# Optimization experiments

Measured on AMD Instinct MI355X. Metric: run time of the kernel, lower is better.

The kernel has to match this reference:

```python
import jax, jax.numpy as jnp
import numpy as np

H = 16          # n_self_heads
CHUNK = 256     # chunk_size in chunk_gate_retention
GLN = 16.0      # gate_logit_normalizer
EPS = 1e-5      # norm_eps


def _rope_interleaved(t, cos, sin):
    # t: [B,T,H,hd]; cos,sin: [T,hd//2]; interleaved pairs (even, odd)
    x1 = t[..., 0::2]
    x2 = t[..., 1::2]
    c = cos[None, :, None, :]
    s = sin[None, :, None, :]
    r1 = x1 * c - x2 * s
    r2 = x1 * s + x2 * c
    return jnp.stack([r1, r2], axis=-1).reshape(t.shape)


def setup_inputs() -> dict:
    key = jax.random.key(0)
    ks = jax.random.split(key, 8)
    B, T, D = 2, 4096, 2048
    hd = D // H
    sc = D ** -0.5
    x = jax.random.normal(ks[0], (B, T, D), jnp.float32)
    # real rotary tables (interleaved), [T, hd//2]
    inv_freq = 1.0 / (10000.0 ** (np.arange(0, hd, 2, dtype=np.float32) / hd))
    ang = np.outer(np.arange(T, dtype=np.float32), inv_freq)
    cos = jnp.asarray(np.cos(ang))
    sin = jnp.asarray(np.sin(ang))
    Wq = jax.random.normal(ks[1], (D, D), jnp.float32) * sc
    Wk = jax.random.normal(ks[2], (D, D), jnp.float32) * sc
    Wv = jax.random.normal(ks[3], (D, D), jnp.float32) * sc
    Wg = jax.random.normal(ks[4], (D, D), jnp.float32) * sc
    Wgt = jax.random.normal(ks[5], (D, H), jnp.float32) * sc
    Wout = jax.random.normal(ks[6], (D, D), jnp.float32) * sc
    return {"x": x, "cos": cos, "sin": sin, "Wq": Wq, "Wk": Wk, "Wv": Wv,
            "Wg": Wg, "Wgt": Wgt, "Wout": Wout}


def reference(x, cos, sin, Wq, Wk, Wv, Wg, Wgt, Wout):
    B, T, D = x.shape
    hd = D // H
    N = T // CHUNK
    scale = hd ** -0.5

    q = (x @ Wq).reshape(B, T, H, hd)
    k = (x @ Wk).reshape(B, T, H, hd)
    v = (x @ Wv).reshape(B, T, H, hd)
    g = x @ Wg                                   # [B,T,D] swiglu gate
    gt = jax.nn.log_sigmoid(x @ Wgt) / GLN       # [B,T,H] log-decay per head

    q = _rope_interleaved(q, cos, sin)
    k = _rope_interleaved(k, cos, sin)

    # chunk: [B,H,N,C,hd]
    def chunked(t):
        return t.transpose(0, 2, 1, 3).reshape(B, H, N, CHUNK, hd)
    qc, kc, vc = chunked(q), chunked(k), chunked(v)

    gtc = gt.transpose(0, 2, 1).reshape(B, H, N, CHUNK).astype(jnp.float32)
    gcum = jnp.cumsum(gtc, axis=-1)              # inclusive cumsum within chunk

    # intra-chunk: A[i,j] = (q_i.k_j)*scale * exp(gcum_i - gcum_j), j <= i
    mask = jnp.tril(jnp.ones((CHUNK, CHUNK), bool))
    dec = jnp.where(mask, jnp.exp(gcum[..., :, None] - gcum[..., None, :]), 0.0).astype(x.dtype)
    scores = jnp.einsum('bhncd,bhnsd->bhncs', qc * scale, kc) * dec
    o_inner = jnp.einsum('bhncs,bhnsd->bhncd', scores, vc)

    # cross-chunk recurrent state: S <- S*exp(g_total) + (k*exp(g_total-gcum))^T V * scale
    g_tot = gcum[..., -1:]                       # [B,H,N,1]
    k_dec = jnp.exp(g_tot - gcum).astype(x.dtype)
    S_in = jnp.einsum('bhncd,bhnce->bhnde', kc * k_dec[..., None] * scale, vc)  # [B,H,N,hd,hd]
    q_dec = jnp.exp(gcum).astype(x.dtype)        # [B,H,N,C]
    chunk_dec = jnp.exp(gcum[..., -1]).astype(x.dtype)  # [B,H,N]

    def step(S, inp):
        qcn, qd, Sin, cd = inp
        o_cross = jnp.einsum('bhcd,bhde->bhce', qcn * qd[..., None], S)
        S_new = S * cd[..., None, None] + Sin
        return S_new, o_cross

    xs = (jnp.moveaxis(qc, 2, 0), jnp.moveaxis(q_dec, 2, 0),
          jnp.moveaxis(S_in, 2, 0), jnp.moveaxis(chunk_dec, 2, 0))
    S0 = jnp.zeros((B, H, hd, hd), x.dtype)
    _, o_cross = jax.lax.scan(step, S0, xs)      # [N,B,H,C,hd]

    o = o_inner + jnp.moveaxis(o_cross, 0, 2)    # [B,H,N,C,hd]
    # RMSNorm over head_dim, no affine
    o = o * jax.lax.rsqrt(jnp.mean(o * o, axis=-1, keepdims=True) + EPS)
    o = o.reshape(B, H, T, hd).transpose(0, 2, 1, 3).reshape(B, T, D)
    o = jax.nn.silu(g) * o                       # swiglu(g, o)
    return o @ Wout
```

## Files before the change

kernel.cpp:

```cpp
#include <hip/hip_runtime.h>

typedef unsigned short u16;
typedef short bf16x8 __attribute__((ext_vector_type(8)));
typedef unsigned short u16x8 __attribute__((ext_vector_type(8)));
typedef unsigned short u16x4 __attribute__((ext_vector_type(4)));
typedef float f32x4 __attribute__((ext_vector_type(4)));

typedef __attribute__((address_space(1))) void* gas_ptr;
typedef __attribute__((address_space(3))) void* las_ptr;

__device__ __forceinline__ float bf2f(u16 v) {
  unsigned u = ((unsigned)v) << 16;
  return __builtin_bit_cast(float, u);
}
__device__ __forceinline__ u16 f2bf(float f) {
  unsigned u = __builtin_bit_cast(unsigned, f);
  u += 0x7fffu + ((u >> 16) & 1u);
  return (u16)(u >> 16);
}
__device__ __forceinline__ f32x4 mfma16(bf16x8 a, bf16x8 b, f32x4 c) {
  return __builtin_amdgcn_mfma_f32_16x16x32_bf16(a, b, c, 0, 0, 0);
}
__device__ __forceinline__ void gload_lds16(const void* g, void* l) {
  __builtin_amdgcn_global_load_lds((gas_ptr)g, (las_ptr)l, 16, 0, 0);
}

#define SB __builtin_amdgcn_sched_barrier(0)
#define BAR do { SB; __builtin_amdgcn_s_barrier(); SB; } while (0)
#define LGK do { asm volatile("s_waitcnt lgkmcnt(0)" ::: "memory"); SB; } while (0)

__global__ void k_cast(const float* __restrict__ in, u16* __restrict__ out, int n8) {
  int stride = gridDim.x * blockDim.x;
  for (int i = blockIdx.x * blockDim.x + threadIdx.x; i < n8; i += stride) {
    size_t base = (size_t)i * 8;
    f32x4 a = *(const f32x4*)(in + base);
    f32x4 b = *(const f32x4*)(in + base + 4);
    u16x8 o;
    o[0] = f2bf(a[0]); o[1] = f2bf(a[1]); o[2] = f2bf(a[2]); o[3] = f2bf(a[3]);
    o[4] = f2bf(b[0]); o[5] = f2bf(b[1]); o[6] = f2bf(b[2]); o[7] = f2bf(b[3]);
    *(u16x8*)(out + base) = o;
  }
}

__global__ __launch_bounds__(256) void k_wtrans(const float* __restrict__ W, u16* __restrict__ WT,
                                                int K, int N) {
  int n0 = blockIdx.x * 64, k0 = blockIdx.y * 64;
  int tid = threadIdx.x;
  __shared__ __align__(16) float tf[64][68];
  int r = tid >> 4, c4 = (tid & 15) * 4;
#pragma unroll
  for (int i = 0; i < 4; ++i) {
    int row = r + i * 16;
    f32x4 v = *(const f32x4*)(W + (size_t)(k0 + row) * N + n0 + c4);
    *(f32x4*)&tf[row][c4] = v;
  }
  __syncthreads();
#pragma unroll
  for (int i = 0; i < 2; ++i) {
    int chunk = tid + i * 256;
    int nl = chunk >> 3, c8 = (chunk & 7) * 8;
    u16x8 o;
#pragma unroll
    for (int m = 0; m < 8; ++m) o[m] = f2bf(tf[c8 + m][nl]);
    *(u16x8*)(WT + (size_t)(n0 + nl) * K + k0 + c8) = o;
  }
}

template <int MODE>
__global__ __launch_bounds__(512, 2) void k_gemm2(const u16* __restrict__ A,
                                                  const u16* __restrict__ Bt,
                                                  void* __restrict__ Cp, int M, int N, int K) {
  __shared__ __align__(16) u16 Al[2][2][8192];
  __shared__ __align__(16) u16 Bl[2][2][8192];
  int tid = threadIdx.x, w = tid >> 6, lane = tid & 63, l15 = lane & 15, l4 = lane >> 4;
  int wm = w >> 2, wn = w & 3;
  int nwg = gridDim.x, bid = blockIdx.x;
  int q8 = nwg >> 3;
  int wg = (bid & 7) * q8 + (bid >> 3);
  int nbx = N >> 8;
  int nstx = nbx >> 2;
  int st = wg >> 4, r16 = wg & 15;
  int sm = st / nstx, sn = st - sm * nstx;
  int m0 = ((sm << 2) + (r16 >> 2)) << 8;
  int n0 = ((sn << 2) + (r16 & 3)) << 8;
  int rA0, rA1, rB0, rB1, cc0, cc1;
  {
    int rr[2], cch[2];
#pragma unroll
    for (int q = 0; q < 2; ++q) {
      int L = (q * 512 + tid) * 16;
      int sub = L >> 10, inner = L & 1023;
      inner ^= ((inner >> 9) & 1) << 5;
      rr[q] = ((sub >> 1) << 4) + (inner >> 6);
      cch[q] = ((sub & 1) << 5) + ((inner & 63) >> 1);
    }
    rA0 = ((rr[0] >> 6) << 7) + (rr[0] & 63);
    rA1 = ((rr[1] >> 6) << 7) + (rr[1] & 63);
    rB0 = ((rr[0] >> 5) << 6) + (rr[0] & 31);
    rB1 = ((rr[1] >> 5) << 6) + (rr[1] & 31);
    cc0 = cch[0]; cc1 = cch[1];
  }
  int innerA = ((l15 << 6) + (l4 << 4)) ^ ((l15 & 8) << 2);
  int ldsW = w << 9;

#define STAGE_A(t, h)                                                                   \
  do {                                                                                  \
    int b_ = (t) & 1;                                                                   \
    gload_lds16(A + (size_t)(m0 + rA0 + (h) * 64) * K + (t) * 64 + cc0, &Al[b_][h][ldsW]); \
    gload_lds16(A + (size_t)(m0 + rA1 + (h) * 64) * K + (t) * 64 + cc1, &Al[b_][h][4096 + ldsW]); \
  } while (0)
#define STAGE_B(t, h)                                                                   \
  do {                                                                                  \
    int b_ = (t) & 1;                                                                   \
    gload_lds16(Bt + (size_t)(n0 + rB0 + (h) * 32) * K + (t) * 64 + cc0, &Bl[b_][h][ldsW]); \
    gload_lds16(Bt + (size_t)(n0 + rB1 + (h) * 32) * K + (t) * 64 + cc1, &Bl[b_][h][4096 + ldsW]); \
  } while (0)

  const f32x4 z4 = {0.f, 0.f, 0.f, 0.f};
  f32x4 acc[8][4];
#pragma unroll
  for (int i = 0; i < 8; ++i)
#pragma unroll
    for (int j = 0; j < 4; ++j) acc[i][j] = z4;
  bf16x8 af[4][2], bfr[2][2][2];

#define LDA(cur, hm)                                                                     \
  do {                                                                                   \
    const char* Ab = (const char*)&Al[cur][hm][0];                                       \
    _Pragma("unroll") for (int fi = 0; fi < 4; ++fi) _Pragma("unroll") for (int ks = 0; ks < 2; ++ks) \
        af[fi][ks] = *(const bf16x8*)(Ab + (((wm * 4 + fi) * 2 + ks) << 10) + innerA);   \
  } while (0)
#define LDB(cur, hn)                                                                     \
  do {                                                                                   \
    const char* Bb = (const char*)&Bl[cur][hn][0];                                       \
    _Pragma("unroll") for (int fj = 0; fj < 2; ++fj) _Pragma("unroll") for (int ks = 0; ks < 2; ++ks) \
        bfr[hn][fj][ks] = *(const bf16x8*)(Bb + (((wn * 2 + fj) * 2 + ks) << 10) + innerA); \
  } while (0)
#define MM(hm, hn)                                                                       \
  do {                                                                                   \
    __builtin_amdgcn_s_setprio(1);                                                       \
    _Pragma("unroll") for (int fi = 0; fi < 4; ++fi) _Pragma("unroll") for (int fj = 0; fj < 2; ++fj) \
        _Pragma("unroll") for (int ks = 0; ks < 2; ++ks)                                 \
            acc[(hm) * 4 + fi][(hn) * 2 + fj] =                                          \
                mfma16(af[fi][ks], bfr[hn][fj][ks], acc[(hm) * 4 + fi][(hn) * 2 + fj]);  \
    __builtin_amdgcn_s_setprio(0);                                                       \
  } while (0)

  int nt = K >> 6;
  STAGE_A(0, 0); STAGE_B(0, 0); STAGE_B(0, 1);
  if (nt > 1) {
    STAGE_A(0, 1); STAGE_A(1, 0); STAGE_B(1, 0);
    asm volatile("s_waitcnt vmcnt(6)" ::: "memory");
  } else {
    STAGE_A(0, 1);
    asm volatile("s_waitcnt vmcnt(0)" ::: "memory");
  }
  SB;
  BAR;
  for (int t = 0; t < nt; ++t) {
    int cur = t & 1;
    LDA(cur, 0); LDB(cur, 0); LDB(cur, 1);
    if (t + 1 < nt) STAGE_B(t + 1, 1);
    BAR; LGK;
    MM(0, 0);
    BAR;
    if (t + 1 < nt) STAGE_A(t + 1, 1);
    MM(0, 1);
    if (t < nt - 1) { asm volatile("s_waitcnt vmcnt(8)" ::: "memory"); }
    else            { asm volatile("s_waitcnt vmcnt(0)" ::: "memory"); }
    SB;
    BAR;
    LDA(cur, 1);
    if (t + 2 < nt) STAGE_A(t + 2, 0);
    BAR; LGK;
    MM(1, 0);
    BAR;
    if (t + 2 < nt) STAGE_B(t + 2, 0);
    MM(1, 1);
    if (t < nt - 2)       { asm volatile("s_waitcnt vmcnt(6)" ::: "memory"); SB; }
    else if (t == nt - 2) { asm volatile("s_waitcnt vmcnt(2)" ::: "memory"); SB; }
    BAR;
  }
  asm volatile("s_waitcnt vmcnt(0)" ::: "memory");
#undef STAGE_A
#undef STAGE_B
#undef LDA
#undef LDB
#undef MM
#pragma unroll
  for (int fi = 0; fi < 8; ++fi)
#pragma unroll
    for (int fj = 0; fj < 4; ++fj) {
      int row = m0 + wm * 128 + fi * 16 + l4 * 4;
      int col = n0 + wn * 64 + fj * 16 + l15;
      if (MODE == 1) {
        float* C = (float*)Cp;
#pragma unroll
        for (int reg = 0; reg < 4; ++reg) C[(size_t)(row + reg) * N + col] = acc[fi][fj][reg];
      } else {
        u16* C = (u16*)Cp + (size_t)(col >> 11) * 16777216 + (col & 2047);
#pragma unroll
        for (int reg = 0; reg < 4; ++reg) C[(size_t)(row + reg) * 2048] = f2bf(acc[fi][fj][reg]);
      }
    }
}

__global__ __launch_bounds__(256) void k_gt(const float* __restrict__ x, const float* __restrict__ Wgt,
                                            float* __restrict__ gt) {
  int t = blockIdx.x, tid = threadIdx.x;
  __shared__ __align__(16) float xs[2048];
#pragma unroll
  for (int i = 0; i < 8; ++i) xs[tid + i * 256] = x[(size_t)t * 2048 + tid + i * 256];
  __syncthreads();
  int head = tid & 15, ks = tid >> 4;
  float p = 0.f;
  for (int i = 0; i < 128; ++i) {
    int k = ks + i * 16;
    p += xs[k] * Wgt[k * 16 + head];
  }
  __shared__ float ps[16][17];
  ps[ks][head] = p;
  __syncthreads();
  if (tid < 16) {
    float z = 0.f;
#pragma unroll
    for (int j = 0; j < 16; ++j) z += ps[j][tid];
    float lsz = (z >= 0.f) ? -log1pf(__expf(-z)) : (z - log1pf(__expf(z)));
    int b = t >> 12, tl = t & 4095;
    gt[((size_t)(b * 16 + tid)) * 4096 + tl] = lsz * 0.0625f;
  }
}

__global__ void k_cumsum(const float* __restrict__ gt, float* __restrict__ gcum) {
  int n = blockIdx.x, bh = blockIdx.y, c = threadIdx.x;
  __shared__ float s[256];
  size_t base = (size_t)bh * 4096 + n * 256;
  s[c] = gt[base + c];
  __syncthreads();
  for (int off = 1; off < 256; off <<= 1) {
    float t = (c >= off) ? s[c - off] : 0.f;
    __syncthreads();
    s[c] += t;
    __syncthreads();
  }
  gcum[base + c] = s[c];
}

__global__ void k_rope(u16* __restrict__ q, u16* __restrict__ k,
                       const float* __restrict__ cosT, const float* __restrict__ sinT) {
  const size_t total = (size_t)8192 * 512;
  size_t stride = (size_t)gridDim.x * blockDim.x;
  for (size_t idx = (size_t)blockIdx.x * blockDim.x + threadIdx.x; idx < total; idx += stride) {
    size_t tok = idx >> 9;
    int g4 = (int)(idx & 511);
    int col = g4 * 4;
    int i0 = (col & 127) >> 1;
    int tl = (int)(tok & 4095);
    float c0 = cosT[tl * 64 + i0], s0 = sinT[tl * 64 + i0];
    float c1 = cosT[tl * 64 + i0 + 1], s1 = sinT[tl * 64 + i0 + 1];
    size_t base = tok * 2048 + col;
    u16x4 qv = *(u16x4*)(q + base);
    float a0 = bf2f(qv[0]), a1 = bf2f(qv[1]), a2 = bf2f(qv[2]), a3 = bf2f(qv[3]);
    u16x4 qo;
    qo[0] = f2bf(a0 * c0 - a1 * s0); qo[1] = f2bf(a0 * s0 + a1 * c0);
    qo[2] = f2bf(a2 * c1 - a3 * s1); qo[3] = f2bf(a2 * s1 + a3 * c1);
    *(u16x4*)(q + base) = qo;
    u16x4 kv = *(u16x4*)(k + base);
    float b0 = bf2f(kv[0]), b1 = bf2f(kv[1]), b2 = bf2f(kv[2]), b3 = bf2f(kv[3]);
    u16x4 ko;
    ko[0] = f2bf(b0 * c0 - b1 * s0); ko[1] = f2bf(b0 * s0 + b1 * c0);
    ko[2] = f2bf(b2 * c1 - b3 * s1); ko[3] = f2bf(b2 * s1 + b3 * c1);
    *(u16x4*)(k + base) = ko;
  }
}

__global__ __launch_bounds__(256) void k_sin(const u16* __restrict__ kb, const u16* __restrict__ vb,
                                             const float* __restrict__ gcum, float* __restrict__ SinT) {
  int n = blockIdx.x, bh = blockIdx.y;
  int b = bh >> 4, h = bh & 15;
  int tid = threadIdx.x, w = tid >> 6, lane = tid & 63, l15 = lane & 15, l4 = lane >> 4;
  size_t t0 = (size_t)b * 4096 + n * 256;
  __shared__ float gc[256];
  __shared__ __align__(16) u16 kt[128 * 72];
  __shared__ __align__(16) u16 vt[128 * 72];
  gc[tid] = gcum[(size_t)bh * 4096 + n * 256 + tid];
  __syncthreads();
  float gtot = gc[255];
  const float scale = 0.08838834764831845f;
  const f32x4 z4 = {0.f, 0.f, 0.f, 0.f};
  f32x4 acc[2][8];
#pragma unroll
  for (int i = 0; i < 2; ++i)
#pragma unroll
    for (int j = 0; j < 8; ++j) acc[i][j] = z4;
  int cl = tid >> 2, fq = (tid & 3) * 32;
  for (int c0 = 0; c0 < 256; c0 += 64) {
    __syncthreads();
    float kd = __expf(gtot - gc[c0 + cl]) * scale;
    const u16* kp = kb + (t0 + c0 + cl) * 2048 + h * 128 + fq;
    const u16* vp = vb + (t0 + c0 + cl) * 2048 + h * 128 + fq;
#pragma unroll
    for (int jj = 0; jj < 4; ++jj) {
      u16x8 kv = *(const u16x8*)(kp + jj * 8);
      u16x8 vv = *(const u16x8*)(vp + jj * 8);
#pragma unroll
      for (int m = 0; m < 8; ++m) {
        int f = fq + jj * 8 + m;
        kt[f * 72 + cl] = f2bf(bf2f(kv[m]) * kd);
        vt[f * 72 + cl] = vv[m];
      }
    }
    __syncthreads();
#pragma unroll
    for (int ks = 0; ks < 2; ++ks) {
      int coff = ks * 32 + l4 * 8;
      bf16x8 bfr[8];
#pragma unroll
      for (int bc = 0; bc < 8; ++bc) bfr[bc] = *(const bf16x8*)(vt + (bc * 16 + l15) * 72 + coff);
#pragma unroll
      for (int ar = 0; ar < 2; ++ar) {
        bf16x8 afr = *(const bf16x8*)(kt + (w * 32 + ar * 16 + l15) * 72 + coff);
#pragma unroll
        for (int bc = 0; bc < 8; ++bc) acc[ar][bc] = mfma16(afr, bfr[bc], acc[ar][bc]);
      }
    }
  }
  size_t sbo = ((size_t)bh * 16 + n) * 16384;
#pragma unroll
  for (int ar = 0; ar < 2; ++ar) {
    int d = w * 32 + ar * 16 + l4 * 4;
#pragma unroll
    for (int bc = 0; bc < 8; ++bc) {
      int e = bc * 16 + l15;
      *(f32x4*)(SinT + sbo + (size_t)e * 128 + d) = acc[ar][bc];
    }
  }
}

__global__ void k_state(const float* __restrict__ SinT, const float* __restrict__ gcum,
                        u16* __restrict__ S_T) {
  int bh = blockIdx.x >> 3, sl = blockIdx.x & 7;
  int base_l = sl * 2048 + threadIdx.x;
  float S[8];
#pragma unroll
  for (int i = 0; i < 8; ++i) S[i] = 0.f;
  for (int nn = 0; nn < 16; ++nn) {
    size_t tb = ((size_t)bh * 16 + nn) * 16384;
#pragma unroll
    for (int i = 0; i < 8; ++i) S_T[tb + base_l + i * 256] = f2bf(S[i]);
    float cd = __expf(gcum[(size_t)bh * 4096 + nn * 256 + 255]);
#pragma unroll
    for (int i = 0; i < 8; ++i) S[i] = S[i] * cd + SinT[tb + base_l + i * 256];
  }
}

__global__ __launch_bounds__(512, 4) void k_attn(
    const u16* __restrict__ qb, const u16* __restrict__ kb, const u16* __restrict__ vb,
    const u16* __restrict__ gbuf, const float* __restrict__ gcum,
    const u16* __restrict__ S_T, u16* __restrict__ ob) {
  int n = blockIdx.x, bh = blockIdx.y;
  int b = bh >> 4, h = bh & 15;
  int tid = threadIdx.x, w = tid >> 6, lane = tid & 63, l15 = lane & 15, l4 = lane >> 4;
  size_t t0 = (size_t)b * 4096 + n * 256;
  __shared__ float gc[256];
  __shared__ __align__(16) u16 vt[32768];
  __shared__ __align__(16) u16 Pb[8][512];
  if (tid < 256) gc[tid] = gcum[(size_t)bh * 4096 + n * 256 + tid];
  {
    int s = tid & 255, e0 = (tid >> 8) * 64;
    const u16* vp = vb + (t0 + s) * 2048 + h * 128 + e0;
#pragma unroll
    for (int j = 0; j < 8; ++j) {
      u16x8 vv = *(const u16x8*)(vp + j * 8);
#pragma unroll
      for (int m = 0; m < 8; ++m) {
        int e = e0 + j * 8 + m;
        vt[(e * 256 + s) ^ ((e & 7) << 3)] = vv[m];
      }
    }
  }
  __syncthreads();
  const float scale = 0.08838834764831845f;
  u16* P = Pb[w];
  const f32x4 z4 = {0.f, 0.f, 0.f, 0.f};
  f32x4 acc[2][8];
#pragma unroll
  for (int i = 0; i < 2; ++i)
#pragma unroll
    for (int j = 0; j < 8; ++j) acc[i][j] = z4;
  int r0s[2], nsbs[2];
  r0s[0] = w * 16;        nsbs[0] = (w + 2) >> 1;
  r0s[1] = (15 - w) * 16; nsbs[1] = 8 - (w >> 1);
#pragma unroll
  for (int rb = 0; rb < 2; ++rb) {
    int r0 = r0s[rb], nsb = nsbs[rb];
    bf16x8 qa[4];
    {
      const u16* qp = qb + (t0 + r0 + l15) * 2048 + h * 128 + l4 * 8;
#pragma unroll
      for (int ks = 0; ks < 4; ++ks) qa[ks] = *(const bf16x8*)(qp + ks * 32);
    }
    for (int sbk = 0; sbk < nsb; ++sbk) {
      int s0 = sbk * 32;
      f32x4 sc[2] = {z4, z4};
#pragma unroll
      for (int cf = 0; cf < 2; ++cf) {
        const u16* kp = kb + (t0 + s0 + cf * 16 + l15) * 2048 + h * 128 + l4 * 8;
#pragma unroll
        for (int ks = 0; ks < 4; ++ks)
          sc[cf] = mfma16(qa[ks], *(const bf16x8*)(kp + ks * 32), sc[cf]);
      }
#pragma unroll
      for (int cf = 0; cf < 2; ++cf) {
        int s = s0 + cf * 16 + l15;
        float gs = gc[s];
#pragma unroll
        for (int reg = 0; reg < 4; ++reg) {
          int rl = l4 * 4 + reg;
          int r = r0 + rl;
          float val = (r >= s) ? sc[cf][reg] * scale * __expf(gc[r] - gs) : 0.f;
          P[(rl * 32 + cf * 16 + l15) ^ ((rl & 3) << 3)] = f2bf(val);
        }
      }
      bf16x8 pa = *(const bf16x8*)(P + ((l15 * 32 + l4 * 8) ^ ((l15 & 3) << 3)));
#pragma unroll
      for (int bc = 0; bc < 8; ++bc) {
        int e = bc * 16 + l15;
        bf16x8 vf = *(const bf16x8*)(vt + ((e * 256 + s0 + l4 * 8) ^ ((e & 7) << 3)));
        acc[rb][bc] = mfma16(pa, vf, acc[rb][bc]);
      }
    }
  }
  size_t sbase = ((size_t)bh * 16 + n) * 16384;
#pragma unroll
  for (int rb = 0; rb < 2; ++rb) {
    int r0 = r0s[rb];
    float qd = __expf(gc[r0 + l15]);
#pragma unroll
    for (int ks = 0; ks < 4; ++ks) {
      u16x8 qu = *(const u16x8*)(qb + (t0 + r0 + l15) * 2048 + h * 128 + ks * 32 + l4 * 8);
      u16x8 ru;
#pragma unroll
      for (int m = 0; m < 8; ++m) ru[m] = f2bf(bf2f(qu[m]) * qd);
      bf16x8 pa2 = __builtin_bit_cast(bf16x8, ru);
#pragma unroll
      for (int bc = 0; bc < 8; ++bc) {
        int e = bc * 16 + l15;
        bf16x8 sf = *(const bf16x8*)(S_T + sbase + (size_t)e * 128 + ks * 32 + l4 * 8);
        acc[rb][bc] = mfma16(pa2, sf, acc[rb][bc]);
      }
    }
  }
#pragma unroll
  for (int rb = 0; rb < 2; ++rb) {
    int r0 = r0s[rb];
#pragma unroll
    for (int reg = 0; reg < 4; ++reg) {
      float ss = 0.f;
#pragma unroll
      for (int bc = 0; bc < 8; ++bc) { float v = acc[rb][bc][reg]; ss += v * v; }
      ss += __shfl_xor(ss, 1);
      ss += __shfl_xor(ss, 2);
      ss += __shfl_xor(ss, 4);
      ss += __shfl_xor(ss, 8);
      float rinv = rsqrtf(ss * 0.0078125f + 1e-5f);
      int r = r0 + l4 * 4 + reg;
      size_t rowoff = (t0 + r) * 2048 + h * 128;
#pragma unroll
      for (int bc = 0; bc < 8; ++bc) {
        int e = bc * 16 + l15;
        float gval = bf2f(gbuf[rowoff + e]);
        float sig = 1.f / (1.f + __expf(-gval));
        ob[rowoff + e] = f2bf(acc[rb][bc][reg] * rinv * gval * sig);
      }
    }
  }
}

extern "C" void kernel_launch(void* const* d_in, const int* in_sizes, int n_in,
                              void* d_out, int out_size, void* d_ws, size_t ws_size,
                              hipStream_t stream) {
  const float* x    = (const float*)d_in[0];
  const float* cosT = (const float*)d_in[1];
  const float* sinT = (const float*)d_in[2];
  const float* Wq   = (const float*)d_in[3];
  const float* Wk   = (const float*)d_in[4];
  const float* Wv   = (const float*)d_in[5];
  const float* Wg   = (const float*)d_in[6];
  const float* Wgt  = (const float*)d_in[7];
  const float* Wout = (const float*)d_in[8];
  float* out = (float*)d_out;

  const size_t MB32 = (size_t)33554432;
  const size_t W8   = (size_t)8388608;
  char* ws = (char*)d_ws;
  size_t need = MB32 + 5 * W8 + 4 * MB32 + 2 * (size_t)524288;
  if (ws_size < need) return;

  u16*   xb    = (u16*)(ws);
  float* SinT  = (float*)(ws);
  u16*   ob    = (u16*)(ws);
  u16*   WqT   = (u16*)(ws + MB32);
  u16*   S_T   = (u16*)(ws + MB32);
  u16*   WoutT = (u16*)(ws + MB32 + 4 * W8);
  u16*   qb    = (u16*)(ws + MB32 + 5 * W8);
  u16*   kb    = qb + 16777216;
  u16*   vb    = qb + 2 * 16777216;
  u16*   gb    = qb + 3 * (size_t)16777216;
  float* gt    = (float*)(ws + MB32 + 5 * W8 + 4 * MB32);
  float* gcum  = (float*)(ws + MB32 + 5 * W8 + 4 * MB32 + 524288);

  k_cast<<<2048, 256, 0, stream>>>(x, xb, 2097152);
  k_wtrans<<<dim3(32, 32), 256, 0, stream>>>(Wq, WqT, 2048, 2048);
  k_wtrans<<<dim3(32, 32), 256, 0, stream>>>(Wk, WqT + 4194304, 2048, 2048);
  k_wtrans<<<dim3(32, 32), 256, 0, stream>>>(Wv, WqT + 2 * 4194304, 2048, 2048);
  k_wtrans<<<dim3(32, 32), 256, 0, stream>>>(Wg, WqT + 3 * (size_t)4194304, 2048, 2048);
  k_wtrans<<<dim3(32, 32), 256, 0, stream>>>(Wout, WoutT, 2048, 2048);

  k_gemm2<2><<<1024, 512, 0, stream>>>(xb, WqT, qb, 8192, 8192, 2048);

  k_gt<<<8192, 256, 0, stream>>>(x, Wgt, gt);
  k_cumsum<<<dim3(16, 32), 256, 0, stream>>>(gt, gcum);
  k_rope<<<4096, 256, 0, stream>>>(qb, kb, cosT, sinT);
  k_sin<<<dim3(16, 32), 256, 0, stream>>>(kb, vb, gcum, SinT);
  k_state<<<256, 256, 0, stream>>>(SinT, gcum, S_T);
  k_attn<<<dim3(16, 32), 512, 0, stream>>>(qb, kb, vb, gb, gcum, S_T, ob);
  k_gemm2<1><<<256, 512, 0, stream>>>(ob, WoutT, out, 8192, 2048, 2048);
}
```

Baseline: 569.4 us.

## Software-pipeline LDS fragment loads in GEMM and merge weight transposes into one launch

The GEMM main loop now splits its A/B register fragments into separate half buffers and issues the LDS reads for the next sub-tile before the current MFMA block. It uses partial lgkmcnt waits instead of full waits and drops several barriers, so LDS latency overlaps matrix math. The five separate weight-transpose launches become one launch that selects the weight by blockIdx.z, which relies on WoutT sitting right after the four concatenated weights. The tighter waitcnt bookkeeping adds register pressure and raises the risk of ordering races.

```diff
diff --git a/kernel.cpp b/kernel.cpp
--- a/kernel.cpp
+++ b/kernel.cpp
@@ -27,7 +27,6 @@
 
 #define SB __builtin_amdgcn_sched_barrier(0)
 #define BAR do { SB; __builtin_amdgcn_s_barrier(); SB; } while (0)
-#define LGK do { asm volatile("s_waitcnt lgkmcnt(0)" ::: "memory"); SB; } while (0)
 
 __global__ void k_cast(const float* __restrict__ in, u16* __restrict__ out, int n8) {
   int stride = gridDim.x * blockDim.x;
@@ -42,8 +41,16 @@
   }
 }
 
-__global__ __launch_bounds__(256) void k_wtrans(const float* __restrict__ W, u16* __restrict__ WT,
-                                                int K, int N) {
+__global__ __launch_bounds__(256) void k_wtrans5(const float* __restrict__ W0,
+                                                 const float* __restrict__ W1,
+                                                 const float* __restrict__ W2,
+                                                 const float* __restrict__ W3,
+                                                 const float* __restrict__ W4,
+                                                 u16* __restrict__ WT) {
+  const int K = 2048, N = 2048;
+  int z = blockIdx.z;
+  const float* W = (z == 0) ? W0 : (z == 1) ? W1 : (z == 2) ? W2 : (z == 3) ? W3 : W4;
+  u16* dst = WT + (size_t)z * 4194304;
   int n0 = blockIdx.x * 64, k0 = blockIdx.y * 64;
   int tid = threadIdx.x;
   __shared__ __align__(16) float tf[64][68];
@@ -62,7 +69,7 @@
     u16x8 o;
 #pragma unroll
     for (int m = 0; m < 8; ++m) o[m] = f2bf(tf[c8 + m][nl]);
-    *(u16x8*)(WT + (size_t)(n0 + nl) * K + k0 + c8) = o;
+    *(u16x8*)(dst + (size_t)(n0 + nl) * K + k0 + c8) = o;
   }
 }
 
@@ -122,70 +129,87 @@
   for (int i = 0; i < 8; ++i)
 #pragma unroll
     for (int j = 0; j < 4; ++j) acc[i][j] = z4;
-  bf16x8 af[4][2], bfr[2][2][2];
-
-#define LDA(cur, hm)                                                                     \
+  bf16x8 af0[4][2], af1[4][2], bf0[2][2], bf1[2][2];
+
+#define LDA0(buf)                                                                        \
   do {                                                                                   \
-    const char* Ab = (const char*)&Al[cur][hm][0];                                       \
+    const char* Ab = (const char*)&Al[buf][0][0];                                        \
     _Pragma("unroll") for (int fi = 0; fi < 4; ++fi) _Pragma("unroll") for (int ks = 0; ks < 2; ++ks) \
-        af[fi][ks] = *(const bf16x8*)(Ab + (((wm * 4 + fi) * 2 + ks) << 10) + innerA);   \
-  } while (0)
-#define LDB(cur, hn)                                                                     \
+        af0[fi][ks] = *(const bf16x8*)(Ab + (((wm * 4 + fi) * 2 + ks) << 10) + innerA);  \
+  } while (0)
+#define LDA1(buf)                                                                        \
   do {                                                                                   \
-    const char* Bb = (const char*)&Bl[cur][hn][0];                                       \
+    const char* Ab = (const char*)&Al[buf][1][0];                                        \
+    _Pragma("unroll") for (int fi = 0; fi < 4; ++fi) _Pragma("unroll") for (int ks = 0; ks < 2; ++ks) \
+        af1[fi][ks] = *(const bf16x8*)(Ab + (((wm * 4 + fi) * 2 + ks) << 10) + innerA);  \
+  } while (0)
+#define LDB0(buf)                                                                        \
+  do {                                                                                   \
+    const char* Bb = (const char*)&Bl[buf][0][0];                                        \
     _Pragma("unroll") for (int fj = 0; fj < 2; ++fj) _Pragma("unroll") for (int ks = 0; ks < 2; ++ks) \
-        bfr[hn][fj][ks] = *(const bf16x8*)(Bb + (((wn * 2 + fj) * 2 + ks) << 10) + innerA); \
-  } while (0)
-#define MM(hm, hn)                                                                       \
+        bf0[fj][ks] = *(const bf16x8*)(Bb + (((wn * 2 + fj) * 2 + ks) << 10) + innerA);  \
+  } while (0)
+#define LDB1(buf)                                                                        \
+  do {                                                                                   \
+    const char* Bb = (const char*)&Bl[buf][1][0];                                        \
+    _Pragma("unroll") for (int fj = 0; fj < 2; ++fj) _Pragma("unroll") for (int ks = 0; ks < 2; ++ks) \
+        bf1[fj][ks] = *(const bf16x8*)(Bb + (((wn * 2 + fj) * 2 + ks) << 10) + innerA);  \
+  } while (0)
+#define MM(hm, hn, AF, BF)                                                               \
   do {                                                                                   \
     __builtin_amdgcn_s_setprio(1);                                                       \
     _Pragma("unroll") for (int fi = 0; fi < 4; ++fi) _Pragma("unroll") for (int fj = 0; fj < 2; ++fj) \
         _Pragma("unroll") for (int ks = 0; ks < 2; ++ks)                                 \
             acc[(hm) * 4 + fi][(hn) * 2 + fj] =                                          \
-                mfma16(af[fi][ks], bfr[hn][fj][ks], acc[(hm) * 4 + fi][(hn) * 2 + fj]);  \
+                mfma16(AF[fi][ks], BF[fj][ks], acc[(hm) * 4 + fi][(hn) * 2 + fj]);       \
     __builtin_amdgcn_s_setprio(0);                                                       \
   } while (0)
 
   int nt = K >> 6;
-  STAGE_A(0, 0); STAGE_B(0, 0); STAGE_B(0, 1);
+  STAGE_A(0, 0); STAGE_B(0, 0); STAGE_A(0, 1); STAGE_B(0, 1);
   if (nt > 1) {
-    STAGE_A(0, 1); STAGE_A(1, 0); STAGE_B(1, 0);
-    asm volatile("s_waitcnt vmcnt(6)" ::: "memory");
+    STAGE_A(1, 0); STAGE_B(1, 0);
+    asm volatile("s_waitcnt vmcnt(4)" ::: "memory");
   } else {
-    STAGE_A(0, 1);
     asm volatile("s_waitcnt vmcnt(0)" ::: "memory");
   }
   SB;
   BAR;
+  LDA0(0); LDB0(0);
   for (int t = 0; t < nt; ++t) {
-    int cur = t & 1;
-    LDA(cur, 0); LDB(cur, 0); LDB(cur, 1);
+    int cur = t & 1, nxt = cur ^ 1;
+    LDB1(cur);
     if (t + 1 < nt) STAGE_B(t + 1, 1);
-    BAR; LGK;
-    MM(0, 0);
+    asm volatile("s_waitcnt lgkmcnt(4)" ::: "memory"); SB;
+    MM(0, 0, af0, bf0);
     BAR;
+    LDA1(cur);
     if (t + 1 < nt) STAGE_A(t + 1, 1);
-    MM(0, 1);
-    if (t < nt - 1) { asm volatile("s_waitcnt vmcnt(8)" ::: "memory"); }
-    else            { asm volatile("s_waitcnt vmcnt(0)" ::: "memory"); }
+    asm volatile("s_waitcnt lgkmcnt(8)" ::: "memory"); SB;
+    MM(0, 1, af0, bf1);
+    BAR;
+    if (t + 2 < nt) STAGE_A(t + 2, 0);
+    asm volatile("s_waitcnt lgkmcnt(0)" ::: "memory"); SB;
+    MM(1, 0, af1, bf0);
+    if (t + 1 < nt) {
+      if (t + 2 < nt) { asm volatile("s_waitcnt vmcnt(6)" ::: "memory"); }
+      else            { asm volatile("s_waitcnt vmcnt(4)" ::: "memory"); }
+    } else            { asm volatile("s_waitcnt vmcnt(0)" ::: "memory"); }
     SB;
     BAR;
-    LDA(cur, 1);
-    if (t + 2 < nt) STAGE_A(t + 2, 0);
-    BAR; LGK;
-    MM(1, 0);
+    if (t + 1 < nt) { LDA0(nxt); LDB0(nxt); }
+    if (t + 2 < nt) STAGE_B(t + 2, 0);
+    MM(1, 1, af1, bf1);
     BAR;
-    if (t + 2 < nt) STAGE_B(t + 2, 0);
-    MM(1, 1);
-    if (t < nt - 2)       { asm volatile("s_waitcnt vmcnt(6)" ::: "memory"); SB; }
-    else if (t == nt - 2) { asm volatile("s_waitcnt vmcnt(2)" ::: "memory"); SB; }
-    BAR;
-  }
+  }
+  asm volatile("s_waitcnt lgkmcnt(0)" ::: "memory");
   asm volatile("s_waitcnt vmcnt(0)" ::: "memory");
 #undef STAGE_A
 #undef STAGE_B
-#undef LDA
-#undef LDB
+#undef LDA0
+#undef LDA1
+#undef LDB0
+#undef LDB1
 #undef MM
 #pragma unroll
   for (int fi = 0; fi < 8; ++fi)
@@ -511,11 +535,7 @@
   float* gcum  = (float*)(ws + MB32 + 5 * W8 + 4 * MB32 + 524288);
 
   k_cast<<<2048, 256, 0, stream>>>(x, xb, 2097152);
-  k_wtrans<<<dim3(32, 32), 256, 0, stream>>>(Wq, WqT, 2048, 2048);
-  k_wtrans<<<dim3(32, 32), 256, 0, stream>>>(Wk, WqT + 4194304, 2048, 2048);
-  k_wtrans<<<dim3(32, 32), 256, 0, stream>>>(Wv, WqT + 2 * 4194304, 2048, 2048);
-  k_wtrans<<<dim3(32, 32), 256, 0, stream>>>(Wg, WqT + 3 * (size_t)4194304, 2048, 2048);
-  k_wtrans<<<dim3(32, 32), 256, 0, stream>>>(Wout, WoutT, 2048, 2048);
+  k_wtrans5<<<dim3(32, 32, 5), 256, 0, stream>>>(Wq, Wk, Wv, Wg, Wout, WqT);
 
   k_gemm2<2><<<1024, 512, 0, stream>>>(xb, WqT, qb, 8192, 8192, 2048);
 
```

Result: faster. 545.4 us (-4.2%).
